# Optimization experiments

Measured on AMD Instinct MI355X. Metric: run time of the kernel, lower is better.

The kernel has to match this reference:

```python
import jax, jax.numpy as jnp
import numpy as np

N_NODES = 100000


def setup_inputs() -> dict:
    key = jax.random.key(0)
    k1, k2, k3, k4, k5 = jax.random.split(key, 5)
    in_f, out_f, E = 128, 128, 1600000
    std = 1.0 / np.sqrt(out_f)
    H = jax.random.normal(k1, (N_NODES, in_f), dtype=jnp.float32)
    W = jax.random.uniform(k2, (in_f, out_f), minval=-std, maxval=std, dtype=jnp.float32)
    bias = jax.random.uniform(k3, (out_f,), minval=-std, maxval=std, dtype=jnp.float32)
    row = jax.random.randint(k4, (E,), 0, N_NODES, dtype=jnp.int32)
    col = jax.random.randint(k5, (E,), 0, N_NODES, dtype=jnp.int32)
    return {"H": H, "W": W, "bias": bias, "row": row, "col": col}


def reference(H, W, bias, row, col):
    # H: [N, in_f]; W: [in_f, out_f]; row/col: [E] edge endpoints
    Hp = jnp.matmul(H, W)  # [N, out_f]
    # edge-wise attention: leaky_relu(<Hp[i], Hp[j]>)
    scores = jax.nn.leaky_relu(jnp.sum(Hp[row] * Hp[col], axis=-1), negative_slope=0.2)  # [E]
    # scatter-softmax over rows (matches sparse_softmax: exp / (row_sum + 1e-10))
    ex = jnp.exp(scores)
    denom = jax.ops.segment_sum(ex, row, num_segments=N_NODES)  # [N]
    attn = ex / (denom[row] + 1e-10)  # [E]
    # sparse-matmul aggregation: out[i] = sum_e attn[e] * Hp[col[e]]
    out = jax.ops.segment_sum(attn[:, None] * Hp[col], row, num_segments=N_NODES)  # [N, out_f]
    return out + bias
```

## Files before the change

kernel.cpp:

```cpp
#include <hip/hip_runtime.h>
#include <hip/hip_bf16.h>

#define RSH 7
#define RPB (1 << RSH)
#define CSH 17
#define CMASK ((1 << CSH) - 1)
#define CHUNK_E 8192
#define CAP 4096

typedef __attribute__((ext_vector_type(8))) _Float16 f16x8;
typedef __attribute__((ext_vector_type(2))) _Float16 f16x2;
typedef __attribute__((ext_vector_type(4))) float f32x4;

struct HL { unsigned int hi, lo; };
__device__ __forceinline__ HL split2(float a, float b) {
    _Float16 ha = (_Float16)a, hb = (_Float16)b;
    _Float16 la = (_Float16)(a - (float)ha), lb = (_Float16)(b - (float)hb);
    union { _Float16 h[2]; unsigned int u; } uh, ul;
    uh.h[0] = ha; uh.h[1] = hb;
    ul.h[0] = la; ul.h[1] = lb;
    HL r; r.hi = uh.u; r.lo = ul.u; return r;
}
__device__ __forceinline__ unsigned short f2h_bits(float f) {
    union { _Float16 h; unsigned short u; } c;
    c.h = (_Float16)f;
    return c.u;
}

__global__ __launch_bounds__(512) void gemm_hist(
    const float* __restrict__ H, const float* __restrict__ Wg,
    unsigned short* __restrict__ Hpb, int N,
    const int* __restrict__ row, unsigned short* __restrict__ Ht,
    int E, int nchunk, int nb2, int gemmBlocks)
{
    __shared__ unsigned short Ahi[128 * 128];
    __shared__ unsigned short Alo[128 * 128];
    __shared__ unsigned short Whi[128 * 128];
    __shared__ unsigned short Wlo[128 * 128];
    const int tid = threadIdx.x;

    if (blockIdx.x >= gemmBlocks) {
        int* cnt = (int*)Ahi;
        const int c = blockIdx.x - gemmBlocks;
        for (int i = tid; i < nb2; i += 512) cnt[i] = 0;
        __syncthreads();
        const int e0 = c * CHUNK_E;
        const int e1 = min(e0 + CHUNK_E, E);
        for (int e = e0 + tid; e < e1; e += 512)
            atomicAdd(&cnt[row[e] >> RSH], 1);
        __syncthreads();
        for (int i = tid; i < nb2; i += 512)
            Ht[(size_t)i * nchunk + c] = (unsigned short)cnt[i];
        return;
    }

    const int rbase = blockIdx.x * 128;

    #pragma unroll
    for (int i = 0; i < 4; ++i) {
        int task = tid + 512 * i;
        int n  = task & 127;
        int k0 = (task >> 7) * 8;
        unsigned int hi[4], lo[4];
        #pragma unroll
        for (int j = 0; j < 4; ++j) {
            float w0 = Wg[(size_t)(k0 + 2*j)     * 128 + n];
            float w1 = Wg[(size_t)(k0 + 2*j + 1) * 128 + n];
            HL s = split2(w0, w1);
            hi[j] = s.hi; lo[j] = s.lo;
        }
        int byte = (k0 * 2) ^ ((n & 7) << 4);
        *(uint4*)((char*)Whi + n * 256 + byte) = make_uint4(hi[0], hi[1], hi[2], hi[3]);
        *(uint4*)((char*)Wlo + n * 256 + byte) = make_uint4(lo[0], lo[1], lo[2], lo[3]);
    }
    #pragma unroll
    for (int i = 0; i < 8; ++i) {
        int flat = tid + 512 * i;
        int rr = flat >> 5;
        int c4  = (flat & 31) * 4;
        float4 h = make_float4(0.f, 0.f, 0.f, 0.f);
        if (rbase + rr < N)
            h = *(const float4*)&H[(size_t)(rbase + rr) * 128 + c4];
        HL s01 = split2(h.x, h.y);
        HL s23 = split2(h.z, h.w);
        uint2 vh, vl;
        vh.x = s01.hi; vh.y = s23.hi;
        vl.x = s01.lo; vl.y = s23.lo;
        int byte = (c4 * 2) ^ ((rr & 7) << 4);
        *(uint2*)((char*)Ahi + rr * 256 + byte) = vh;
        *(uint2*)((char*)Alo + rr * 256 + byte) = vl;
    }
    __syncthreads();

    const int wid = tid >> 6, lane = tid & 63;
    const int wm = wid >> 1, wn = wid & 1;
    const int lr = lane & 15, lg = lane >> 4;
    f32x4 acc[2][4] = {};

    #pragma unroll
    for (int ks = 0; ks < 4; ++ks) {
        const int kb = ks * 64 + lg * 16;
        f16x8 ahi[2], alo[2];
        #pragma unroll
        for (int mi = 0; mi < 2; ++mi) {
            int rr = wm * 32 + mi * 16 + lr;
            int sw = kb ^ ((rr & 7) << 4);
            ahi[mi] = *(const f16x8*)((char*)Ahi + rr * 256 + sw);
            alo[mi] = *(const f16x8*)((char*)Alo + rr * 256 + sw);
        }
        #pragma unroll
        for (int nf = 0; nf < 4; ++nf) {
            int n = wn * 64 + nf * 16 + lr;
            int sw = kb ^ ((n & 7) << 4);
            f16x8 bhi = *(const f16x8*)((char*)Whi + n * 256 + sw);
            f16x8 blo = *(const f16x8*)((char*)Wlo + n * 256 + sw);
            #pragma unroll
            for (int mi = 0; mi < 2; ++mi) {
                acc[mi][nf] = __builtin_amdgcn_mfma_f32_16x16x32_f16(ahi[mi], bhi, acc[mi][nf], 0, 0, 0);
                acc[mi][nf] = __builtin_amdgcn_mfma_f32_16x16x32_f16(ahi[mi], blo, acc[mi][nf], 0, 0, 0);
                acc[mi][nf] = __builtin_amdgcn_mfma_f32_16x16x32_f16(alo[mi], bhi, acc[mi][nf], 0, 0, 0);
            }
        }
    }

    #pragma unroll
    for (int mi = 0; mi < 2; ++mi) {
        #pragma unroll
        for (int nf = 0; nf < 4; ++nf) {
            int col = wn * 64 + nf * 16 + lr;
            #pragma unroll
            for (int i = 0; i < 4; ++i) {
                int rr = rbase + wm * 32 + mi * 16 + lg * 4 + i;
                if (rr < N)
                    Hpb[(size_t)rr * 128 + col] = f2h_bits(acc[mi][nf][i]);
            }
        }
    }
}

__global__ __launch_bounds__(256) void bucket_scan(
    const unsigned short* __restrict__ Ht, unsigned short* __restrict__ rel,
    int* __restrict__ totals, int nchunk)
{
    __shared__ int s[256];
    const int b = blockIdx.x, tid = threadIdx.x;
    int v = (tid < nchunk) ? (int)Ht[(size_t)b * nchunk + tid] : 0;
    s[tid] = v;
    __syncthreads();
    for (int d = 1; d < 256; d <<= 1) {
        int t = (tid >= d) ? s[tid - d] : 0;
        __syncthreads();
        s[tid] += t;
        __syncthreads();
    }
    if (tid < nchunk) rel[(size_t)b * nchunk + tid] = (unsigned short)(s[tid] - v);
    if (tid == 255) totals[b] = s[255];
}

__global__ __launch_bounds__(1024) void bucket_ptr_scan(
    const int* __restrict__ totals, int* __restrict__ bucketptr, int nb2)
{
    __shared__ int s[1024];
    const int tid = threadIdx.x;
    int v = (tid < nb2) ? totals[tid] : 0;
    s[tid] = v;
    __syncthreads();
    for (int d = 1; d < 1024; d <<= 1) {
        int t = (tid >= d) ? s[tid - d] : 0;
        __syncthreads();
        s[tid] += t;
        __syncthreads();
    }
    if (tid < nb2) bucketptr[tid] = s[tid] - v;
    if (tid == nb2 - 1) bucketptr[nb2] = s[tid];
}

__global__ __launch_bounds__(256) void chunk_scatter(
    const int* __restrict__ row, const int* __restrict__ col,
    const unsigned short* __restrict__ rel, const int* __restrict__ bucketptr,
    int* __restrict__ colsort, int E, int nchunk, int nb2)
{
    __shared__ int loc[1025];
    __shared__ int cur[1024];
    __shared__ int gb[1024];
    __shared__ unsigned short bid[CHUNK_E];
    __shared__ int ord[CHUNK_E];
    __shared__ int part[256];
    const int tid = threadIdx.x;
    const int c = blockIdx.x;
    const int e0 = c * CHUNK_E;
    const int tot = min(CHUNK_E, E - e0);

    for (int i = tid; i < nb2; i += 256) loc[i] = 0;
    __syncthreads();
    for (int j = tid; j < tot; j += 256)
        atomicAdd(&loc[row[e0 + j] >> RSH], 1);
    __syncthreads();

    const int base = tid * 4;
    int v[4]; int s = 0;
    #pragma unroll
    for (int i = 0; i < 4; ++i) {
        int idx = base + i;
        v[i] = (idx < nb2) ? loc[idx] : 0;
        s += v[i];
    }
    part[tid] = s;
    __syncthreads();
    for (int d = 1; d < 256; d <<= 1) {
        int t = (tid >= d) ? part[tid - d] : 0;
        __syncthreads();
        part[tid] += t;
        __syncthreads();
    }
    int run = part[tid] - s;
    #pragma unroll
    for (int i = 0; i < 4; ++i) {
        int idx = base + i;
        if (idx < nb2) { loc[idx] = run; cur[idx] = run; }
        run += v[i];
    }
    if (tid == 255) loc[nb2] = part[255];
    __syncthreads();

    for (int b = tid; b < nb2; b += 256) {
        gb[b] = bucketptr[b] + (int)rel[(size_t)b * nchunk + c];
        int st = loc[b], en = loc[b + 1];
        for (int j = st; j < en; ++j) bid[j] = (unsigned short)b;
    }
    __syncthreads();

    for (int j = tid; j < tot; j += 256) {
        int r = row[e0 + j], cc = col[e0 + j];
        int b = r >> RSH;
        int p = atomicAdd(&cur[b], 1);
        ord[p] = ((r & (RPB - 1)) << CSH) | cc;
    }
    __syncthreads();

    for (int j = tid; j < tot; j += 256) {
        int b = bid[j];
        colsort[gb[b] + (j - loc[b])] = ord[j];
    }
}

__global__ __launch_bounds__(256) void bucket_sort(
    const int* __restrict__ bucketptr, int* __restrict__ rowptr,
    int* __restrict__ colsort, int N)
{
    __shared__ int rcnt[RPB];
    __shared__ int rcur[RPB];
    __shared__ int sc[256];
    __shared__ int ord[CAP];
    const int b = blockIdx.x, tid = threadIdx.x;
    const int rbase = b << RSH;
    const int s0 = bucketptr[b];
    const int cnt = bucketptr[b + 1] - s0;

    if (tid < RPB) rcnt[tid] = 0;
    __syncthreads();
    for (int j = tid; j < cnt; j += 256)
        atomicAdd(&rcnt[colsort[s0 + j] >> CSH], 1);
    __syncthreads();

    int v = (tid < RPB) ? rcnt[tid] : 0;
    sc[tid] = v;
    __syncthreads();
    for (int d = 1; d < RPB; d <<= 1) {
        int t = (tid >= d) ? sc[tid - d] : 0;
        __syncthreads();
        sc[tid] += t;
        __syncthreads();
    }
    if (tid < RPB) {
        int ex = sc[tid] - v;
        rcur[tid] = ex;
        int r = rbase + tid;
        if (r < N) rowptr[r] = s0 + ex;
    }
    if (tid == RPB - 1) {
        int rend = min(rbase + RPB, N);
        rowptr[rend] = s0 + cnt;
    }
    __syncthreads();

    for (int j = tid; j < cnt; j += 256) {
        int rec = colsort[s0 + j];
        int p = atomicAdd(&rcur[rec >> CSH], 1);
        ord[p] = rec & CMASK;
    }
    __syncthreads();
    for (int j = tid; j < cnt; j += 256)
        colsort[s0 + j] = ord[j];
}

union F16x8U {
    uint4 v;
    f16x2 p[4];
    _Float16 h[8];
};

__device__ __forceinline__ float dot8(const f16x2* a, const F16x8U& b) {
#if __has_builtin(__builtin_amdgcn_fdot2)
    float d = __builtin_amdgcn_fdot2(a[0], b.p[0], 0.f, false);
    d = __builtin_amdgcn_fdot2(a[1], b.p[1], d, false);
    d = __builtin_amdgcn_fdot2(a[2], b.p[2], d, false);
    d = __builtin_amdgcn_fdot2(a[3], b.p[3], d, false);
    return d;
#else
    float d = 0.f;
    #pragma unroll
    for (int k = 0; k < 8; ++k)
        d = fmaf((float)a[k >> 1][k & 1], (float)b.h[k], d);
    return d;
#endif
}

__global__ __launch_bounds__(256) void aggregate_kernel(
    const unsigned short* __restrict__ Hpb, const int* __restrict__ rowptr,
    const int* __restrict__ cols, const float* __restrict__ bias,
    float* __restrict__ out, int N)
{
    const int lane = threadIdx.x & 63;
    const int wv   = threadIdx.x >> 6;
    const int r = blockIdx.x * 4 + wv;
    if (r >= N) return;
    const int d = lane & 15;
    const int g = lane >> 4;

    const float4* bp = (const float4*)&bias[d * 8];
    const float4 b0 = bp[0], b1 = bp[1];

    F16x8U hru;
    hru.v = *(const uint4*)&Hpb[(size_t)r * 128 + d * 8];
    f16x2 hr2[4] = {hru.p[0], hru.p[1], hru.p[2], hru.p[3]};

    float acc[8] = {0.f,0.f,0.f,0.f,0.f,0.f,0.f,0.f};
    float den = 0.f;
    const int e0 = rowptr[r], e1 = rowptr[r + 1];
    const int elast = e1 - 1;

    for (int e = e0 + g; e < e1; e += 8) {
        const bool m1 = (e + 4 < e1);
        const int eb = m1 ? e + 4 : elast;
        int c0 = cols[e];
        int c1 = cols[eb];
        F16x8U u0, u1;
        u0.v = *(const uint4*)&Hpb[(size_t)c0 * 128 + d * 8];
        u1.v = *(const uint4*)&Hpb[(size_t)c1 * 128 + d * 8];

        float dot0 = dot8(hr2, u0);
        float dot1 = dot8(hr2, u1);

        dot0 += __shfl_xor(dot0, 1);
        dot1 += __shfl_xor(dot1, 1);
        dot0 += __shfl_xor(dot0, 2);
        dot1 += __shfl_xor(dot1, 2);
        dot0 += __shfl_xor(dot0, 4);
        dot1 += __shfl_xor(dot1, 4);
        dot0 += __shfl_xor(dot0, 8);
        dot1 += __shfl_xor(dot1, 8);

        float s0 = fmaxf(dot0, 0.2f * dot0);
        float s1 = fmaxf(dot1, 0.2f * dot1);
        float ex0 = __expf(s0);
        float ex1 = m1 ? __expf(s1) : 0.f;
        den += ex0 + ex1;
        #pragma unroll
        for (int k = 0; k < 8; ++k) {
            acc[k] = fmaf((float)u0.h[k], ex0, acc[k]);
            acc[k] = fmaf((float)u1.h[k], ex1, acc[k]);
        }
    }

    #pragma unroll
    for (int k = 0; k < 8; ++k) {
        acc[k] += __shfl_xor(acc[k], 16);
        acc[k] += __shfl_xor(acc[k], 32);
    }
    den += __shfl_xor(den, 16);
    den += __shfl_xor(den, 32);

    if (g == 0) {
        float inv = 1.f / (den + 1e-10f);
        float4 o0, o1;
        o0.x = fmaf(acc[0], inv, b0.x);
        o0.y = fmaf(acc[1], inv, b0.y);
        o0.z = fmaf(acc[2], inv, b0.z);
        o0.w = fmaf(acc[3], inv, b0.w);
        o1.x = fmaf(acc[4], inv, b1.x);
        o1.y = fmaf(acc[5], inv, b1.y);
        o1.z = fmaf(acc[6], inv, b1.z);
        o1.w = fmaf(acc[7], inv, b1.w);
        float4* op = (float4*)&out[(size_t)r * 128 + d * 8];
        op[0] = o0;
        op[1] = o1;
    }
}

extern "C" void kernel_launch(void* const* d_in, const int* in_sizes, int n_in,
                              void* d_out, int out_size, void* d_ws, size_t ws_size,
                              hipStream_t stream)
{
    const float* H    = (const float*)d_in[0];
    const float* W    = (const float*)d_in[1];
    const float* bias = (const float*)d_in[2];
    const int*   row  = (const int*)d_in[3];
    const int*   col  = (const int*)d_in[4];
    const int N = in_sizes[0] / 128;
    const int E = in_sizes[3];

    const int nchunk = (E + CHUNK_E - 1) / CHUNK_E;
    const int nb2    = (N + RPB - 1) / RPB;

    auto align = [](size_t x) { return (x + 255) & ~(size_t)255; };

    char* ws = (char*)d_ws;
    size_t off = 0;
    unsigned short* Hpb       = (unsigned short*)(ws + off); off = align(off + (size_t)N * 128 * 2);
    unsigned short* Ht        = (unsigned short*)(ws + off); off = align(off + (size_t)nb2 * nchunk * 2);
    unsigned short* rel       = (unsigned short*)(ws + off); off = align(off + (size_t)nb2 * nchunk * 2);
    int*            totals    = (int*)(ws + off);            off = align(off + (size_t)nb2 * 4);
    int*            bucketptr = (int*)(ws + off);            off = align(off + (size_t)(nb2 + 1) * 4);
    int*            rowptr    = (int*)(ws + off);            off = align(off + (size_t)(N + 1) * 4);
    int*            colsort   = (int*)(ws + off);

    const int gemmBlocks = (N + 127) / 128;

    gemm_hist<<<gemmBlocks + nchunk, 512, 0, stream>>>(H, W, Hpb, N,
                                                       row, Ht, E, nchunk, nb2,
                                                       gemmBlocks);
    bucket_scan<<<nb2, 256, 0, stream>>>(Ht, rel, totals, nchunk);
    bucket_ptr_scan<<<1, 1024, 0, stream>>>(totals, bucketptr, nb2);
    chunk_scatter<<<nchunk, 256, 0, stream>>>(row, col, rel, bucketptr,
                                              colsort, E, nchunk, nb2);
    bucket_sort<<<nb2, 256, 0, stream>>>(bucketptr, rowptr, colsort, N);
    aggregate_kernel<<<(N + 3) / 4, 256, 0, stream>>>(Hpb, rowptr, colsort, bias,
                                                      (float*)d_out, N);
}
```

Baseline: 138.9 us.

## Precompute W fp16 split once and simplify chunk scatter to direct atomic writes

Adds a small kernel that splits W into swizzled fp16 hi/lo arrays once in global memory. GEMM blocks then copy these instead of each recomputing the split from strided fp32 loads. The chunk_scatter kernel drops its per-chunk histogram, scan and shared-memory staging, and writes entries directly to colsort at an atomically assigned offset within each bucket. This cuts LDS use and barriers, but the global writes become scattered and the order within a bucket becomes nondeterministic; the later per-bucket sort is relied on to handle that.

```diff
diff --git a/kernel.cpp b/kernel.cpp
--- a/kernel.cpp
+++ b/kernel.cpp
@@ -7,6 +7,7 @@
 #define CMASK ((1 << CSH) - 1)
 #define CHUNK_E 8192
 #define CAP 4096
+#define NBMAX 1024
 
 typedef __attribute__((ext_vector_type(8))) _Float16 f16x8;
 typedef __attribute__((ext_vector_type(2))) _Float16 f16x2;
@@ -27,8 +28,30 @@
     return c.u;
 }
 
+__global__ __launch_bounds__(256) void wsplit(
+    const float* __restrict__ Wg, unsigned int* __restrict__ WhiG,
+    unsigned int* __restrict__ WloG)
+{
+    int task = blockIdx.x * 256 + threadIdx.x;
+    if (task >= 2048) return;
+    int n  = task & 127;
+    int k0 = (task >> 7) * 8;
+    unsigned int hi[4], lo[4];
+    #pragma unroll
+    for (int j = 0; j < 4; ++j) {
+        float w0 = Wg[(size_t)(k0 + 2*j)     * 128 + n];
+        float w1 = Wg[(size_t)(k0 + 2*j + 1) * 128 + n];
+        HL s = split2(w0, w1);
+        hi[j] = s.hi; lo[j] = s.lo;
+    }
+    int byte = (k0 * 2) ^ ((n & 7) << 4);
+    *(uint4*)((char*)WhiG + n * 256 + byte) = make_uint4(hi[0], hi[1], hi[2], hi[3]);
+    *(uint4*)((char*)WloG + n * 256 + byte) = make_uint4(lo[0], lo[1], lo[2], lo[3]);
+}
+
 __global__ __launch_bounds__(512) void gemm_hist(
-    const float* __restrict__ H, const float* __restrict__ Wg,
+    const float* __restrict__ H,
+    const unsigned int* __restrict__ WhiG, const unsigned int* __restrict__ WloG,
     unsigned short* __restrict__ Hpb, int N,
     const int* __restrict__ row, unsigned short* __restrict__ Ht,
     int E, int nchunk, int nb2, int gemmBlocks)
@@ -58,20 +81,9 @@
 
     #pragma unroll
     for (int i = 0; i < 4; ++i) {
-        int task = tid + 512 * i;
-        int n  = task & 127;
-        int k0 = (task >> 7) * 8;
-        unsigned int hi[4], lo[4];
-        #pragma unroll
-        for (int j = 0; j < 4; ++j) {
-            float w0 = Wg[(size_t)(k0 + 2*j)     * 128 + n];
-            float w1 = Wg[(size_t)(k0 + 2*j + 1) * 128 + n];
-            HL s = split2(w0, w1);
-            hi[j] = s.hi; lo[j] = s.lo;
-        }
-        int byte = (k0 * 2) ^ ((n & 7) << 4);
-        *(uint4*)((char*)Whi + n * 256 + byte) = make_uint4(hi[0], hi[1], hi[2], hi[3]);
-        *(uint4*)((char*)Wlo + n * 256 + byte) = make_uint4(lo[0], lo[1], lo[2], lo[3]);
+        int idx = tid + 512 * i;
+        ((uint4*)Whi)[idx] = ((const uint4*)WhiG)[idx];
+        ((uint4*)Wlo)[idx] = ((const uint4*)WloG)[idx];
     }
     #pragma unroll
     for (int i = 0; i < 8; ++i) {
@@ -180,53 +192,16 @@
     const unsigned short* __restrict__ rel, const int* __restrict__ bucketptr,
     int* __restrict__ colsort, int E, int nchunk, int nb2)
 {
-    __shared__ int loc[1025];
-    __shared__ int cur[1024];
-    __shared__ int gb[1024];
-    __shared__ unsigned short bid[CHUNK_E];
-    __shared__ int ord[CHUNK_E];
-    __shared__ int part[256];
+    __shared__ int cur[NBMAX];
+    __shared__ int gb[NBMAX];
     const int tid = threadIdx.x;
     const int c = blockIdx.x;
     const int e0 = c * CHUNK_E;
     const int tot = min(CHUNK_E, E - e0);
 
-    for (int i = tid; i < nb2; i += 256) loc[i] = 0;
-    __syncthreads();
-    for (int j = tid; j < tot; j += 256)
-        atomicAdd(&loc[row[e0 + j] >> RSH], 1);
-    __syncthreads();
-
-    const int base = tid * 4;
-    int v[4]; int s = 0;
-    #pragma unroll
-    for (int i = 0; i < 4; ++i) {
-        int idx = base + i;
-        v[i] = (idx < nb2) ? loc[idx] : 0;
-        s += v[i];
-    }
-    part[tid] = s;
-    __syncthreads();
-    for (int d = 1; d < 256; d <<= 1) {
-        int t = (tid >= d) ? part[tid - d] : 0;
-        __syncthreads();
-        part[tid] += t;
-        __syncthreads();
-    }
-    int run = part[tid] - s;
-    #pragma unroll
-    for (int i = 0; i < 4; ++i) {
-        int idx = base + i;
-        if (idx < nb2) { loc[idx] = run; cur[idx] = run; }
-        run += v[i];
-    }
-    if (tid == 255) loc[nb2] = part[255];
-    __syncthreads();
-
     for (int b = tid; b < nb2; b += 256) {
+        cur[b] = 0;
         gb[b] = bucketptr[b] + (int)rel[(size_t)b * nchunk + c];
-        int st = loc[b], en = loc[b + 1];
-        for (int j = st; j < en; ++j) bid[j] = (unsigned short)b;
     }
     __syncthreads();
 
@@ -234,13 +209,7 @@
         int r = row[e0 + j], cc = col[e0 + j];
         int b = r >> RSH;
         int p = atomicAdd(&cur[b], 1);
-        ord[p] = ((r & (RPB - 1)) << CSH) | cc;
-    }
-    __syncthreads();
-
-    for (int j = tid; j < tot; j += 256) {
-        int b = bid[j];
-        colsort[gb[b] + (j - loc[b])] = ord[j];
+        colsort[gb[b] + p] = ((r & (RPB - 1)) << CSH) | cc;
     }
 }
 
@@ -423,11 +392,14 @@
     int*            totals    = (int*)(ws + off);            off = align(off + (size_t)nb2 * 4);
     int*            bucketptr = (int*)(ws + off);            off = align(off + (size_t)(nb2 + 1) * 4);
     int*            rowptr    = (int*)(ws + off);            off = align(off + (size_t)(N + 1) * 4);
+    unsigned int*   WhiG      = (unsigned int*)(ws + off);   off = align(off + 8192 * 4);
+    unsigned int*   WloG      = (unsigned int*)(ws + off);   off = align(off + 8192 * 4);
     int*            colsort   = (int*)(ws + off);
 
     const int gemmBlocks = (N + 127) / 128;
 
-    gemm_hist<<<gemmBlocks + nchunk, 512, 0, stream>>>(H, W, Hpb, N,
+    wsplit<<<8, 256, 0, stream>>>(W, WhiG, WloG);
+    gemm_hist<<<gemmBlocks + nchunk, 512, 0, stream>>>(H, WhiG, WloG, Hpb, N,
                                                        row, Ht, E, nchunk, nb2,
                                                        gemmBlocks);
     bucket_scan<<<nb2, 256, 0, stream>>>(Ht, rel, totals, nchunk);
```

New measurement: 134.8 us. -3.0%, faster.
